# Optimization experiments

Measured on AMD Instinct MI355X. Metric: run time of the kernel, lower is better.

Reference implementation:

```python
import jax, jax.numpy as jnp
import numpy as np

HEAD_DIM = 256
HIDDEN = 1536
INTERMEDIATE = 6144
NUM_KV_HEADS = 1
NUM_Q_HEADS = 8
SCALE = HEAD_DIM ** (-0.5)
PAST_LEN = 8191


def setup_inputs() -> dict:
    key = jax.random.key(0)
    ks = jax.random.split(key, 20)
    def lin(ki, fan_in, fan_out):
        # torch nn.Linear init: U(-1/sqrt(fan_in), 1/sqrt(fan_in)); stored (in, out) for x @ W
        bound = 1.0 / np.sqrt(fan_in)
        W = jax.random.uniform(ki, (fan_in, fan_out), jnp.float32, -bound, bound)
        b = jax.random.uniform(jax.random.fold_in(ki, 1), (fan_out,), jnp.float32, -bound, bound)
        return W, b
    Wq, bq = lin(ks[0], HIDDEN, NUM_Q_HEADS * HEAD_DIM)
    Wk, bk = lin(ks[1], HIDDEN, NUM_KV_HEADS * HEAD_DIM)
    Wv, bv = lin(ks[2], HIDDEN, NUM_KV_HEADS * HEAD_DIM)
    Wo, bo = lin(ks[3], NUM_Q_HEADS * HEAD_DIM, HIDDEN)
    Wg, bg = lin(ks[4], HIDDEN, INTERMEDIATE)
    Wu, bu = lin(ks[5], HIDDEN, INTERMEDIATE)
    Wd, bd = lin(ks[6], INTERMEDIATE, HIDDEN)
    x = jax.random.normal(ks[7], (1, 1, HIDDEN), jnp.float32)
    k_past = jax.random.normal(ks[8], (1, NUM_KV_HEADS, PAST_LEN, HEAD_DIM), jnp.float32)
    v_past = jax.random.normal(ks[9], (1, NUM_KV_HEADS, PAST_LEN, HEAD_DIM), jnp.float32)
    return dict(x=x, k_past=k_past, v_past=v_past,
                Wq=Wq, bq=bq, Wk=Wk, bk=bk, Wv=Wv, bv=bv, Wo=Wo, bo=bo,
                Wg=Wg, bg=bg, Wu=Wu, bu=bu, Wd=Wd, bd=bd)


def reference(x, k_past, v_past, Wq, bq, Wk, bk, Wv, bv, Wo, bo, Wg, bg, Wu, bu, Wd, bd):
    residual = x
    # projections; q: (1, Hq, 1, D), k/v: (1, Hkv, 1, D)
    q = (x @ Wq + bq).reshape(1, 1, NUM_Q_HEADS, HEAD_DIM).transpose(0, 2, 1, 3)
    k = (x @ Wk + bk).reshape(1, 1, NUM_KV_HEADS, HEAD_DIM).transpose(0, 2, 1, 3)
    v = (x @ Wv + bv).reshape(1, 1, NUM_KV_HEADS, HEAD_DIM).transpose(0, 2, 1, 3)
    k_full = jnp.concatenate([k_past, k], axis=2)  # (1, Hkv, S, D)
    v_full = jnp.concatenate([v_past, v], axis=2)
    # GQA: broadcast the single KV head across 8 Q heads (no materialized repeat)
    scores = jnp.einsum('bhqd,bksd->bhqs', q, k_full) * SCALE  # (1, Hq, 1, S)
    attn = jax.nn.softmax(scores, axis=-1)
    out = jnp.einsum('bhqs,bksd->bhqd', attn, v_full)  # (1, Hq, 1, D)
    out = out.transpose(0, 2, 1, 3).reshape(1, 1, NUM_Q_HEADS * HEAD_DIM)
    out = out @ Wo + bo
    x = residual + out
    # MLP: GELU(gate) * up -> down (exact erf GELU, matching torch nn.GELU default)
    ffn = (jax.nn.gelu(x @ Wg + bg, approximate=False) * (x @ Wu + bu)) @ Wd + bd
    return x + ffn
```

## Files before the change

### kernel.cpp

```cpp
#include <hip/hip_runtime.h>
#include <hip/hip_bf16.h>
#include <math.h>

#define PAST 8191
#define SCALEF 0.0625f

using bf = __hip_bfloat16;

__device__ __forceinline__ float bf2f(unsigned short u) {
    return __uint_as_float(((unsigned)u) << 16);
}
__device__ __forceinline__ void unpack8(uint4 r, float* f) {
    f[0] = __uint_as_float(r.x << 16);
    f[1] = __uint_as_float(r.x & 0xffff0000u);
    f[2] = __uint_as_float(r.y << 16);
    f[3] = __uint_as_float(r.y & 0xffff0000u);
    f[4] = __uint_as_float(r.z << 16);
    f[5] = __uint_as_float(r.z & 0xffff0000u);
    f[6] = __uint_as_float(r.w << 16);
    f[7] = __uint_as_float(r.w & 0xffff0000u);
}

template<bool BF16>
__device__ __forceinline__ void load8(const void* W, size_t off, float* f) {
    if constexpr (BF16) {
        uint4 r = *reinterpret_cast<const uint4*>((const unsigned short*)W + off);
        unpack8(r, f);
    } else {
        const float* p = (const float*)W + off;
        float4 a = *reinterpret_cast<const float4*>(p);
        float4 b = *reinterpret_cast<const float4*>(p + 4);
        f[0]=a.x; f[1]=a.y; f[2]=a.z; f[3]=a.w;
        f[4]=b.x; f[5]=b.y; f[6]=b.z; f[7]=b.w;
    }
}
template<bool BF16>
__device__ __forceinline__ void load4(const void* P, size_t off, float* f) {
    if constexpr (BF16) {
        uint2 r = *reinterpret_cast<const uint2*>((const unsigned short*)P + off);
        f[0] = __uint_as_float(r.x << 16); f[1] = __uint_as_float(r.x & 0xffff0000u);
        f[2] = __uint_as_float(r.y << 16); f[3] = __uint_as_float(r.y & 0xffff0000u);
    } else {
        float4 a = *reinterpret_cast<const float4*>((const float*)P + off);
        f[0]=a.x; f[1]=a.y; f[2]=a.z; f[3]=a.w;
    }
}
template<bool BF16>
__device__ __forceinline__ float load1(const void* P, int i) {
    if constexpr (BF16) return bf2f(((const unsigned short*)P)[i]);
    else return ((const float*)P)[i];
}

__global__ __launch_bounds__(256) void probe_kernel(const unsigned int* __restrict__ xw,
                                                    float* __restrict__ zws,
                                                    int* __restrict__ flag) {
    int idx = blockIdx.x * 256 + threadIdx.x;
    #pragma unroll
    for (int k = idx; k < 20480; k += 10240) zws[k] = 0.f;
    if (blockIdx.x == 0) {
        __shared__ int cnt;
        if (threadIdx.x == 0) cnt = 0;
        __syncthreads();
        int ok = 0;
        for (int i = threadIdx.x; i < 768; i += 256) {
            unsigned e = (xw[i] >> 7) & 0xff;
            if (e >= 96 && e <= 142) ok++;
        }
        atomicAdd(&cnt, ok);
        __syncthreads();
        if (threadIdx.x == 0) *flag = (cnt > 500) ? 1 : 0;
    }
}

template<bool BF16>
__device__ __forceinline__ void gemv_rows32(const void* __restrict__ W, int ldw,
                                            const float* __restrict__ xs_wave,
                                            int row0, int j, float acc[8]) {
    #pragma unroll
    for (int i = 0; i < 32; i += 8) {
        float f[8][8];
        #pragma unroll
        for (int r = 0; r < 8; ++r)
            load8<BF16>(W, (size_t)(row0 + i + r) * ldw + j, f[r]);
        #pragma unroll
        for (int r = 0; r < 8; ++r) {
            float xv = xs_wave[i + r];
            #pragma unroll
            for (int q = 0; q < 8; ++q) acc[q] = fmaf(xv, f[r][q], acc[q]);
        }
    }
}

__device__ __forceinline__ void block_reduce_512(float acc[8], float* red,
                                                 int wave, int lane) {
    if (wave > 0) {
        float* dst = red + (wave - 1) * 512 + lane * 8;
        #pragma unroll
        for (int q = 0; q < 8; ++q) dst[q] = acc[q];
    }
    __syncthreads();
    if (wave == 0) {
        int o = lane * 8;
        #pragma unroll
        for (int q = 0; q < 8; ++q)
            acc[q] += red[o + q] + red[512 + o + q] + red[1024 + o + q];
    }
}

template<bool BF16>
__device__ void qkv_body(const void* __restrict__ x, const void* __restrict__ Wq,
                         const void* __restrict__ bq, const void* __restrict__ Wk,
                         const void* __restrict__ bk, const void* __restrict__ Wv,
                         const void* __restrict__ bv, float* __restrict__ qkv) {
    __shared__ float xs[128];
    __shared__ float red[3 * 512];
    int tid = threadIdx.x, wave = tid >> 6, lane = tid & 63;
    int i0 = blockIdx.y * 128;
    if (tid < 128) xs[tid] = load1<BF16>(x, i0 + tid);
    __syncthreads();
    int j = blockIdx.x * 512 + lane * 8;
    const void* W; const void* bias; int ldw, jl;
    if (j < 2048)      { W = Wq; bias = bq; ldw = 2048; jl = j; }
    else if (j < 2304) { W = Wk; bias = bk; ldw = 256;  jl = j - 2048; }
    else               { W = Wv; bias = bv; ldw = 256;  jl = j - 2304; }
    float acc[8] = {0,0,0,0,0,0,0,0};
    gemv_rows32<BF16>(W, ldw, xs + wave * 32, i0 + wave * 32, jl, acc);
    block_reduce_512(acc, red, wave, lane);
    if (wave == 0) {
        if (blockIdx.y == 0) {
            #pragma unroll
            for (int q = 0; q < 8; ++q) acc[q] += load1<BF16>(bias, jl + q);
        }
        #pragma unroll
        for (int q = 0; q < 8; ++q) atomicAdd(&qkv[j + q], acc[q]);
    }
}
__global__ __launch_bounds__(256) void qkv_kernel(
    const void* x, const void* Wq, const void* bq, const void* Wk, const void* bk,
    const void* Wv, const void* bv, float* qkv, const int* flag) {
    if (*flag) qkv_body<true>(x, Wq, bq, Wk, bk, Wv, bv, qkv);
    else       qkv_body<false>(x, Wq, bq, Wk, bk, Wv, bv, qkv);
}

template<bool BF16>
__device__ void attn_body(const float* __restrict__ qkv, const void* __restrict__ k_past,
                          const void* __restrict__ v_past, float* __restrict__ attnout,
                          float* __restrict__ lpart) {
    __shared__ float wsum[8];
    __shared__ float red[3 * 2048];
    int tid = threadIdx.x, wave = tid >> 6, lane = tid & 63;
    if (tid < 8) wsum[tid] = 0.f;
    int d0 = lane * 4;
    float4 qreg[8];
    #pragma unroll
    for (int h = 0; h < 8; ++h)
        qreg[h] = *reinterpret_cast<const float4*>(qkv + h * 256 + d0);
    float4 knew = *reinterpret_cast<const float4*>(qkv + 2048 + d0);
    float4 vnew = *reinterpret_cast<const float4*>(qkv + 2304 + d0);
    __syncthreads();

    float o[8][4];
    #pragma unroll
    for (int h = 0; h < 8; ++h)
        #pragma unroll
        for (int r = 0; r < 4; ++r) o[h][r] = 0.f;
    float wl[8] = {0,0,0,0,0,0,0,0};

    int p0 = blockIdx.x * 64 + wave * 16;
    for (int it = 0; it < 16; it += 8) {
        float kf[8][4], vf[8][4];
        if (p0 + it + 7 < PAST) {
            #pragma unroll
            for (int r = 0; r < 8; ++r)
                load4<BF16>(k_past, (size_t)(p0 + it + r) * 256 + d0, kf[r]);
            #pragma unroll
            for (int r = 0; r < 8; ++r)
                load4<BF16>(v_past, (size_t)(p0 + it + r) * 256 + d0, vf[r]);
        } else {
            #pragma unroll
            for (int r = 0; r < 8; ++r) {
                int p = p0 + it + r;
                if (p < PAST) {
                    load4<BF16>(k_past, (size_t)p * 256 + d0, kf[r]);
                    load4<BF16>(v_past, (size_t)p * 256 + d0, vf[r]);
                } else {
                    kf[r][0]=knew.x; kf[r][1]=knew.y; kf[r][2]=knew.z; kf[r][3]=knew.w;
                    vf[r][0]=vnew.x; vf[r][1]=vnew.y; vf[r][2]=vnew.z; vf[r][3]=vnew.w;
                }
            }
        }
        #pragma unroll
        for (int r = 0; r < 8; ++r) {
            float part[8];
            #pragma unroll
            for (int h = 0; h < 8; ++h) {
                part[h] = qreg[h].x*kf[r][0] + qreg[h].y*kf[r][1]
                        + qreg[h].z*kf[r][2] + qreg[h].w*kf[r][3];
            }
            #pragma unroll
            for (int m = 1; m < 64; m <<= 1) {
                #pragma unroll
                for (int h = 0; h < 8; ++h) part[h] += __shfl_xor(part[h], m, 64);
            }
            #pragma unroll
            for (int h = 0; h < 8; ++h) {
                float w = expf(part[h] * SCALEF);
                wl[h] += w;
                #pragma unroll
                for (int rr = 0; rr < 4; ++rr) o[h][rr] = fmaf(w, vf[r][rr], o[h][rr]);
            }
        }
    }
    if (lane == 0) {
        #pragma unroll
        for (int h = 0; h < 8; ++h) atomicAdd(&wsum[h], wl[h]);
    }
    if (wave > 0) {
        float* dst = red + (wave - 1) * 2048;
        #pragma unroll
        for (int h = 0; h < 8; ++h)
            #pragma unroll
            for (int r = 0; r < 4; ++r) dst[h * 256 + d0 + r] = o[h][r];
    }
    __syncthreads();
    if (wave == 0) {
        #pragma unroll
        for (int h = 0; h < 8; ++h)
            #pragma unroll
            for (int r = 0; r < 4; ++r) {
                float v = o[h][r] + red[h*256 + d0 + r] + red[2048 + h*256 + d0 + r]
                        + red[4096 + h*256 + d0 + r];
                atomicAdd(&attnout[h * 256 + d0 + r], v);
            }
    }
    if (tid < 8) atomicAdd(&lpart[tid * 64 + (blockIdx.x & 63)], wsum[tid]);
}
__global__ __launch_bounds__(256) void attn_kernel(
    const float* qkv, const void* k_past, const void* v_past, float* attnout,
    float* lpart, const int* flag) {
    if (*flag) attn_body<true>(qkv, k_past, v_past, attnout, lpart);
    else       attn_body<false>(qkv, k_past, v_past, attnout, lpart);
}

template<bool BF16>
__device__ void oproj_body(const float* __restrict__ attnout, const float* __restrict__ lpart,
                           const void* __restrict__ Wo, const void* __restrict__ bo,
                           const void* __restrict__ xin, float* __restrict__ x2) {
    __shared__ float xs[128];
    __shared__ float red[3 * 512];
    int tid = threadIdx.x, wave = tid >> 6, lane = tid & 63;
    int i0 = blockIdx.y * 128;
    int h = i0 >> 8;
    if (tid < 128) {
        float v = lpart[h * 64 + (tid & 63)];
        #pragma unroll
        for (int m = 1; m < 64; m <<= 1) v += __shfl_xor(v, m, 64);
        xs[tid] = attnout[i0 + tid] * (1.0f / v);
    }
    __syncthreads();
    int j = blockIdx.x * 512 + lane * 8;
    float acc[8] = {0,0,0,0,0,0,0,0};
    gemv_rows32<BF16>(Wo, 1536, xs + wave * 32, i0 + wave * 32, j, acc);
    block_reduce_512(acc, red, wave, lane);
    if (wave == 0) {
        if (blockIdx.y == 0) {
            #pragma unroll
            for (int q = 0; q < 8; ++q)
                acc[q] += load1<BF16>(bo, j + q) + load1<BF16>(xin, j + q);
        }
        #pragma unroll
        for (int q = 0; q < 8; ++q) atomicAdd(&x2[j + q], acc[q]);
    }
}
__global__ __launch_bounds__(256) void oproj_kernel(
    const float* attnout, const float* lpart, const void* Wo, const void* bo,
    const void* xin, float* x2, const int* flag) {
    if (*flag) oproj_body<true>(attnout, lpart, Wo, bo, xin, x2);
    else       oproj_body<false>(attnout, lpart, Wo, bo, xin, x2);
}

template<bool BF16>
__device__ void gateup_body(const float* __restrict__ x2, const void* __restrict__ Wg,
                            const void* __restrict__ Wu, float* __restrict__ gacc,
                            float* __restrict__ uacc) {
    __shared__ float xs[128];
    __shared__ float red[3 * 512];
    int tid = threadIdx.x, wave = tid >> 6, lane = tid & 63;
    int i0 = blockIdx.y * 128;
    if (tid < 128) xs[tid] = x2[i0 + tid];
    __syncthreads();
    const void* W = blockIdx.z ? Wu : Wg;
    float* out = blockIdx.z ? uacc : gacc;
    int j = blockIdx.x * 512 + lane * 8;
    float acc[8] = {0,0,0,0,0,0,0,0};
    gemv_rows32<BF16>(W, 6144, xs + wave * 32, i0 + wave * 32, j, acc);
    block_reduce_512(acc, red, wave, lane);
    if (wave == 0) {
        #pragma unroll
        for (int q = 0; q < 8; ++q) atomicAdd(&out[j + q], acc[q]);
    }
}
__global__ __launch_bounds__(256) void gateup_kernel(
    const float* x2, const void* Wg, const void* Wu, float* gacc, float* uacc,
    const int* flag) {
    if (*flag) gateup_body<true>(x2, Wg, Wu, gacc, uacc);
    else       gateup_body<false>(x2, Wg, Wu, gacc, uacc);
}

template<bool BF16>
__device__ void down_body(const float* __restrict__ gacc, const float* __restrict__ uacc,
                          const void* __restrict__ bg, const void* __restrict__ bu,
                          const void* __restrict__ Wd, float* __restrict__ yacc) {
    __shared__ float xs[128];
    __shared__ float red[3 * 512];
    int tid = threadIdx.x, wave = tid >> 6, lane = tid & 63;
    int i0 = blockIdx.y * 128;
    if (tid < 128) {
        int i = i0 + tid;
        float g = gacc[i] + load1<BF16>(bg, i);
        float u = uacc[i] + load1<BF16>(bu, i);
        float ge = 0.5f * g * (1.0f + erff(g * 0.70710678118654752f));
        xs[tid] = ge * u;
    }
    __syncthreads();
    int j = blockIdx.x * 512 + lane * 8;
    float acc[8] = {0,0,0,0,0,0,0,0};
    gemv_rows32<BF16>(Wd, 1536, xs + wave * 32, i0 + wave * 32, j, acc);
    block_reduce_512(acc, red, wave, lane);
    if (wave == 0) {
        #pragma unroll
        for (int q = 0; q < 8; ++q) atomicAdd(&yacc[j + q], acc[q]);
    }
}
__global__ __launch_bounds__(256) void down_kernel(
    const float* gacc, const float* uacc, const void* bg, const void* bu,
    const void* Wd, float* yacc, const int* flag) {
    if (*flag) down_body<true>(gacc, uacc, bg, bu, Wd, yacc);
    else       down_body<false>(gacc, uacc, bg, bu, Wd, yacc);
}

__global__ __launch_bounds__(256) void final_kernel(
    const float* __restrict__ x2, const float* __restrict__ yacc,
    const void* __restrict__ bd, void* __restrict__ out, const int* __restrict__ flag) {
    int j = blockIdx.x * 256 + threadIdx.x;
    if (j < 1536) {
        int isbf = *flag;
        float b = isbf ? bf2f(((const unsigned short*)bd)[j]) : ((const float*)bd)[j];
        float v = x2[j] + yacc[j] + b;
        if (isbf) ((bf*)out)[j] = __float2bfloat16(v);
        else      ((float*)out)[j] = v;
    }
}

extern "C" void kernel_launch(void* const* d_in, const int* in_sizes, int n_in,
                              void* d_out, int out_size, void* d_ws, size_t ws_size,
                              hipStream_t stream) {
    const void* x  = d_in[0];
    const void* kp = d_in[1];
    const void* vp = d_in[2];
    const void* Wq = d_in[3];
    const void* bq = d_in[4];
    const void* Wk = d_in[5];
    const void* bk = d_in[6];
    const void* Wv = d_in[7];
    const void* bv = d_in[8];
    const void* Wo = d_in[9];
    const void* bo = d_in[10];
    const void* Wg = d_in[11];
    const void* bg = d_in[12];
    const void* Wu = d_in[13];
    const void* bu = d_in[14];
    const void* Wd = d_in[15];
    const void* bd = d_in[16];

    float* ws      = (float*)d_ws;
    float* qkv     = ws;
    float* x2      = ws + 2560;
    float* gacc    = ws + 4096;
    float* uacc    = ws + 10240;
    float* yacc    = ws + 16384;
    float* attnout = ws + 17920;
    float* lpart   = ws + 19968;
    int*  flag     = (int*)(ws + 86016);

    probe_kernel<<<40, 256, 0, stream>>>((const unsigned int*)x, ws, flag);

    qkv_kernel<<<dim3(5, 12), 256, 0, stream>>>(x, Wq, bq, Wk, bk, Wv, bv, qkv, flag);
    attn_kernel<<<128, 256, 0, stream>>>(qkv, kp, vp, attnout, lpart, flag);
    oproj_kernel<<<dim3(3, 16), 256, 0, stream>>>(attnout, lpart, Wo, bo, x, x2, flag);
    gateup_kernel<<<dim3(12, 12, 2), 256, 0, stream>>>(x2, Wg, Wu, gacc, uacc, flag);
    down_kernel<<<dim3(3, 48), 256, 0, stream>>>(gacc, uacc, bg, bu, Wd, yacc, flag);
    final_kernel<<<6, 256, 0, stream>>>(x2, yacc, bd, d_out, flag);
}
```

Baseline: 270.1 us.

## Halve GEMV row chunks, double grid, split atomic targets, batch attention shuffles

```diff
diff --git a/kernel.cpp b/kernel.cpp
--- a/kernel.cpp
+++ b/kernel.cpp
@@ -55,8 +55,7 @@
                                                     float* __restrict__ zws,
                                                     int* __restrict__ flag) {
     int idx = blockIdx.x * 256 + threadIdx.x;
-    #pragma unroll
-    for (int k = idx; k < 20480; k += 10240) zws[k] = 0.f;
+    for (int k = idx; k < 38400; k += 10240) zws[k] = 0.f;
     if (blockIdx.x == 0) {
         __shared__ int cnt;
         if (threadIdx.x == 0) cnt = 0;
@@ -73,11 +72,11 @@
 }
 
 template<bool BF16>
-__device__ __forceinline__ void gemv_rows32(const void* __restrict__ W, int ldw,
+__device__ __forceinline__ void gemv_rows16(const void* __restrict__ W, int ldw,
                                             const float* __restrict__ xs_wave,
                                             int row0, int j, float acc[8]) {
     #pragma unroll
-    for (int i = 0; i < 32; i += 8) {
+    for (int i = 0; i < 16; i += 8) {
         float f[8][8];
         #pragma unroll
         for (int r = 0; r < 8; ++r)
@@ -112,11 +111,11 @@
                          const void* __restrict__ bq, const void* __restrict__ Wk,
                          const void* __restrict__ bk, const void* __restrict__ Wv,
                          const void* __restrict__ bv, float* __restrict__ qkv) {
-    __shared__ float xs[128];
+    __shared__ float xs[64];
     __shared__ float red[3 * 512];
     int tid = threadIdx.x, wave = tid >> 6, lane = tid & 63;
-    int i0 = blockIdx.y * 128;
-    if (tid < 128) xs[tid] = load1<BF16>(x, i0 + tid);
+    int i0 = blockIdx.y * 64;
+    if (tid < 64) xs[tid] = load1<BF16>(x, i0 + tid);
     __syncthreads();
     int j = blockIdx.x * 512 + lane * 8;
     const void* W; const void* bias; int ldw, jl;
@@ -124,15 +123,16 @@
     else if (j < 2304) { W = Wk; bias = bk; ldw = 256;  jl = j - 2048; }
     else               { W = Wv; bias = bv; ldw = 256;  jl = j - 2304; }
     float acc[8] = {0,0,0,0,0,0,0,0};
-    gemv_rows32<BF16>(W, ldw, xs + wave * 32, i0 + wave * 32, jl, acc);
+    gemv_rows16<BF16>(W, ldw, xs + wave * 16, i0 + wave * 16, jl, acc);
     block_reduce_512(acc, red, wave, lane);
     if (wave == 0) {
         if (blockIdx.y == 0) {
             #pragma unroll
             for (int q = 0; q < 8; ++q) acc[q] += load1<BF16>(bias, jl + q);
         }
-        #pragma unroll
-        for (int q = 0; q < 8; ++q) atomicAdd(&qkv[j + q], acc[q]);
+        float* out = qkv + (blockIdx.y & 1) * 2560;
+        #pragma unroll
+        for (int q = 0; q < 8; ++q) atomicAdd(&out[j + q], acc[q]);
     }
 }
 __global__ __launch_bounds__(256) void qkv_kernel(
@@ -151,12 +151,21 @@
     int tid = threadIdx.x, wave = tid >> 6, lane = tid & 63;
     if (tid < 8) wsum[tid] = 0.f;
     int d0 = lane * 4;
+    const float* qkv1 = qkv + 2560;
     float4 qreg[8];
     #pragma unroll
-    for (int h = 0; h < 8; ++h)
-        qreg[h] = *reinterpret_cast<const float4*>(qkv + h * 256 + d0);
-    float4 knew = *reinterpret_cast<const float4*>(qkv + 2048 + d0);
-    float4 vnew = *reinterpret_cast<const float4*>(qkv + 2304 + d0);
+    for (int h = 0; h < 8; ++h) {
+        float4 a = *reinterpret_cast<const float4*>(qkv + h * 256 + d0);
+        float4 b = *reinterpret_cast<const float4*>(qkv1 + h * 256 + d0);
+        qreg[h].x = a.x + b.x; qreg[h].y = a.y + b.y;
+        qreg[h].z = a.z + b.z; qreg[h].w = a.w + b.w;
+    }
+    float4 ka = *reinterpret_cast<const float4*>(qkv + 2048 + d0);
+    float4 kb = *reinterpret_cast<const float4*>(qkv1 + 2048 + d0);
+    float4 va = *reinterpret_cast<const float4*>(qkv + 2304 + d0);
+    float4 vb = *reinterpret_cast<const float4*>(qkv1 + 2304 + d0);
+    float knew[4] = {ka.x+kb.x, ka.y+kb.y, ka.z+kb.z, ka.w+kb.w};
+    float vnew[4] = {va.x+vb.x, va.y+vb.y, va.z+vb.z, va.w+vb.w};
     __syncthreads();
 
     float o[8][4];
@@ -184,32 +193,35 @@
                     load4<BF16>(k_past, (size_t)p * 256 + d0, kf[r]);
                     load4<BF16>(v_past, (size_t)p * 256 + d0, vf[r]);
                 } else {
-                    kf[r][0]=knew.x; kf[r][1]=knew.y; kf[r][2]=knew.z; kf[r][3]=knew.w;
-                    vf[r][0]=vnew.x; vf[r][1]=vnew.y; vf[r][2]=vnew.z; vf[r][3]=vnew.w;
+                    kf[r][0]=knew[0]; kf[r][1]=knew[1]; kf[r][2]=knew[2]; kf[r][3]=knew[3];
+                    vf[r][0]=vnew[0]; vf[r][1]=vnew[1]; vf[r][2]=vnew[2]; vf[r][3]=vnew[3];
                 }
             }
         }
-        #pragma unroll
-        for (int r = 0; r < 8; ++r) {
-            float part[8];
+        float part[8][8];
+        #pragma unroll
+        for (int r = 0; r < 8; ++r)
+            #pragma unroll
+            for (int h = 0; h < 8; ++h)
+                part[r][h] = qreg[h].x*kf[r][0] + qreg[h].y*kf[r][1]
+                           + qreg[h].z*kf[r][2] + qreg[h].w*kf[r][3];
+        #pragma unroll
+        for (int m = 1; m < 64; m <<= 1) {
+            #pragma unroll
+            for (int r = 0; r < 8; ++r)
+                #pragma unroll
+                for (int h = 0; h < 8; ++h)
+                    part[r][h] += __shfl_xor(part[r][h], m, 64);
+        }
+        #pragma unroll
+        for (int r = 0; r < 8; ++r)
             #pragma unroll
             for (int h = 0; h < 8; ++h) {
-                part[h] = qreg[h].x*kf[r][0] + qreg[h].y*kf[r][1]
-                        + qreg[h].z*kf[r][2] + qreg[h].w*kf[r][3];
-            }
-            #pragma unroll
-            for (int m = 1; m < 64; m <<= 1) {
-                #pragma unroll
-                for (int h = 0; h < 8; ++h) part[h] += __shfl_xor(part[h], m, 64);
-            }
-            #pragma unroll
-            for (int h = 0; h < 8; ++h) {
-                float w = expf(part[h] * SCALEF);
+                float w = expf(part[r][h] * SCALEF);
                 wl[h] += w;
                 #pragma unroll
                 for (int rr = 0; rr < 4; ++rr) o[h][rr] = fmaf(w, vf[r][rr], o[h][rr]);
             }
-        }
     }
     if (lane == 0) {
         #pragma unroll
@@ -246,13 +258,13 @@
 __device__ void oproj_body(const float* __restrict__ attnout, const float* __restrict__ lpart,
                            const void* __restrict__ Wo, const void* __restrict__ bo,
                            const void* __restrict__ xin, float* __restrict__ x2) {
-    __shared__ float xs[128];
+    __shared__ float xs[64];
     __shared__ float red[3 * 512];
     int tid = threadIdx.x, wave = tid >> 6, lane = tid & 63;
-    int i0 = blockIdx.y * 128;
+    int i0 = blockIdx.y * 64;
     int h = i0 >> 8;
-    if (tid < 128) {
-        float v = lpart[h * 64 + (tid & 63)];
+    if (tid < 64) {
+        float v = lpart[h * 64 + tid];
         #pragma unroll
         for (int m = 1; m < 64; m <<= 1) v += __shfl_xor(v, m, 64);
         xs[tid] = attnout[i0 + tid] * (1.0f / v);
@@ -260,7 +272,7 @@
     __syncthreads();
     int j = blockIdx.x * 512 + lane * 8;
     float acc[8] = {0,0,0,0,0,0,0,0};
-    gemv_rows32<BF16>(Wo, 1536, xs + wave * 32, i0 + wave * 32, j, acc);
+    gemv_rows16<BF16>(Wo, 1536, xs + wave * 16, i0 + wave * 16, j, acc);
     block_reduce_512(acc, red, wave, lane);
     if (wave == 0) {
         if (blockIdx.y == 0) {
@@ -268,8 +280,9 @@
             for (int q = 0; q < 8; ++q)
                 acc[q] += load1<BF16>(bo, j + q) + load1<BF16>(xin, j + q);
         }
-        #pragma unroll
-        for (int q = 0; q < 8; ++q) atomicAdd(&x2[j + q], acc[q]);
+        float* out = x2 + (blockIdx.y & 1) * 1536;
+        #pragma unroll
+        for (int q = 0; q < 8; ++q) atomicAdd(&out[j + q], acc[q]);
     }
 }
 __global__ __launch_bounds__(256) void oproj_kernel(
@@ -283,17 +296,17 @@
 __device__ void gateup_body(const float* __restrict__ x2, const void* __restrict__ Wg,
                             const void* __restrict__ Wu, float* __restrict__ gacc,
                             float* __restrict__ uacc) {
-    __shared__ float xs[128];
+    __shared__ float xs[64];
     __shared__ float red[3 * 512];
     int tid = threadIdx.x, wave = tid >> 6, lane = tid & 63;
-    int i0 = blockIdx.y * 128;
-    if (tid < 128) xs[tid] = x2[i0 + tid];
+    int i0 = blockIdx.y * 64;
+    if (tid < 64) xs[tid] = x2[i0 + tid] + x2[1536 + i0 + tid];
     __syncthreads();
     const void* W = blockIdx.z ? Wu : Wg;
-    float* out = blockIdx.z ? uacc : gacc;
+    float* out = (blockIdx.z ? uacc : gacc) + (blockIdx.y & 1) * 6144;
     int j = blockIdx.x * 512 + lane * 8;
     float acc[8] = {0,0,0,0,0,0,0,0};
-    gemv_rows32<BF16>(W, 6144, xs + wave * 32, i0 + wave * 32, j, acc);
+    gemv_rows16<BF16>(W, 6144, xs + wave * 16, i0 + wave * 16, j, acc);
     block_reduce_512(acc, red, wave, lane);
     if (wave == 0) {
         #pragma unroll
@@ -311,25 +324,26 @@
 __device__ void down_body(const float* __restrict__ gacc, const float* __restrict__ uacc,
                           const void* __restrict__ bg, const void* __restrict__ bu,
                           const void* __restrict__ Wd, float* __restrict__ yacc) {
-    __shared__ float xs[128];
+    __shared__ float xs[64];
     __shared__ float red[3 * 512];
     int tid = threadIdx.x, wave = tid >> 6, lane = tid & 63;
-    int i0 = blockIdx.y * 128;
-    if (tid < 128) {
+    int i0 = blockIdx.y * 64;
+    if (tid < 64) {
         int i = i0 + tid;
-        float g = gacc[i] + load1<BF16>(bg, i);
-        float u = uacc[i] + load1<BF16>(bu, i);
+        float g = gacc[i] + gacc[6144 + i] + load1<BF16>(bg, i);
+        float u = uacc[i] + uacc[6144 + i] + load1<BF16>(bu, i);
         float ge = 0.5f * g * (1.0f + erff(g * 0.70710678118654752f));
         xs[tid] = ge * u;
     }
     __syncthreads();
     int j = blockIdx.x * 512 + lane * 8;
     float acc[8] = {0,0,0,0,0,0,0,0};
-    gemv_rows32<BF16>(Wd, 1536, xs + wave * 32, i0 + wave * 32, j, acc);
+    gemv_rows16<BF16>(Wd, 1536, xs + wave * 16, i0 + wave * 16, j, acc);
     block_reduce_512(acc, red, wave, lane);
     if (wave == 0) {
-        #pragma unroll
-        for (int q = 0; q < 8; ++q) atomicAdd(&yacc[j + q], acc[q]);
+        float* out = yacc + (blockIdx.y & 1) * 1536;
+        #pragma unroll
+        for (int q = 0; q < 8; ++q) atomicAdd(&out[j + q], acc[q]);
     }
 }
 __global__ __launch_bounds__(256) void down_kernel(
@@ -346,7 +360,7 @@
     if (j < 1536) {
         int isbf = *flag;
         float b = isbf ? bf2f(((const unsigned short*)bd)[j]) : ((const float*)bd)[j];
-        float v = x2[j] + yacc[j] + b;
+        float v = x2[j] + x2[1536 + j] + yacc[j] + yacc[1536 + j] + b;
         if (isbf) ((bf*)out)[j] = __float2bfloat16(v);
         else      ((float*)out)[j] = v;
     }
@@ -375,20 +389,20 @@
 
     float* ws      = (float*)d_ws;
     float* qkv     = ws;
-    float* x2      = ws + 2560;
-    float* gacc    = ws + 4096;
-    float* uacc    = ws + 10240;
-    float* yacc    = ws + 16384;
-    float* attnout = ws + 17920;
-    float* lpart   = ws + 19968;
-    int*  flag     = (int*)(ws + 86016);
+    float* x2      = ws + 5120;
+    float* gacc    = ws + 8192;
+    float* uacc    = ws + 20480;
+    float* yacc    = ws + 32768;
+    float* attnout = ws + 35840;
+    float* lpart   = ws + 37888;
+    int*  flag     = (int*)(ws + 40960);
 
     probe_kernel<<<40, 256, 0, stream>>>((const unsigned int*)x, ws, flag);
 
-    qkv_kernel<<<dim3(5, 12), 256, 0, stream>>>(x, Wq, bq, Wk, bk, Wv, bv, qkv, flag);
+    qkv_kernel<<<dim3(5, 24), 256, 0, stream>>>(x, Wq, bq, Wk, bk, Wv, bv, qkv, flag);
     attn_kernel<<<128, 256, 0, stream>>>(qkv, kp, vp, attnout, lpart, flag);
-    oproj_kernel<<<dim3(3, 16), 256, 0, stream>>>(attnout, lpart, Wo, bo, x, x2, flag);
-    gateup_kernel<<<dim3(12, 12, 2), 256, 0, stream>>>(x2, Wg, Wu, gacc, uacc, flag);
-    down_kernel<<<dim3(3, 48), 256, 0, stream>>>(gacc, uacc, bg, bu, Wd, yacc, flag);
+    oproj_kernel<<<dim3(3, 32), 256, 0, stream>>>(attnout, lpart, Wo, bo, x, x2, flag);
+    gateup_kernel<<<dim3(12, 24, 2), 256, 0, stream>>>(x2, Wg, Wu, gacc, uacc, flag);
+    down_kernel<<<dim3(3, 96), 256, 0, stream>>>(gacc, uacc, bg, bu, Wd, yacc, flag);
     final_kernel<<<6, 256, 0, stream>>>(x2, yacc, bd, d_out, flag);
 }
```

Measured after the change: 262.1 us. 1.03x faster.
